# Kernel optimization log

Measured on AMD Instinct MI355X. Metric: run time of the kernel, lower is better.

Reference implementation:

```python
import jax, jax.numpy as jnp
import numpy as np

B, S, E, D, H = 32, 4096, 512, 512, 512


def setup_inputs() -> dict:
    key = jax.random.key(0)
    ks = jax.random.split(key, 7)
    scale = 1.0 / np.sqrt(H)
    return {
        "encoder_hiddens": jax.random.normal(ks[0], (B, S, E), dtype=jnp.float32),
        "decoder_hidden": jax.random.normal(ks[1], (B, D), dtype=jnp.float32),
        "W_enc": jax.random.uniform(ks[2], (H, E), jnp.float32, -scale, scale),
        "b_enc": jax.random.uniform(ks[3], (H,), jnp.float32, -scale, scale),
        "W_dec": jax.random.uniform(ks[4], (H, D), jnp.float32, -scale, scale),
        "b_dec": jax.random.uniform(ks[5], (H,), jnp.float32, -scale, scale),
        "v": jax.random.uniform(ks[6], (H,), jnp.float32, -scale, scale),
    }


def reference(encoder_hiddens, decoder_hidden, W_enc, b_enc, W_dec, b_dec, v):
    # Projections (the two small GEMMs of the original per-timestep loop, batched)
    enc_hs = jnp.einsum("bse,he->bsh", encoder_hiddens, W_enc) + b_enc  # [B,S,H]
    dec_h = decoder_hidden @ W_dec.T + b_dec                            # [B,H]

    # Ragged-length detection: the torch loop breaks at the first all-zero
    # projected encoder row; positions at/after that are excluded (cumulative AND).
    nonzero = jnp.any(enc_hs != 0, axis=-1)                             # [B,S]
    valid = jnp.cumprod(nonzero.astype(jnp.int32), axis=1).astype(bool)

    # Additive (Bahdanau) scores: v . tanh(enc_hs + dec_h)
    scores = jnp.einsum("h,bsh->bs", v, jnp.tanh(enc_hs + dec_h[:, None, :]))
    scores = jnp.where(valid, scores, -jnp.inf)
    attn = jax.nn.softmax(scores, axis=1)                               # [B,S]
    attn = jnp.where(valid, attn, 0.0)

    # Weighted sum of encoder states -> context vector [B,1,E]
    return jnp.sum(encoder_hiddens * attn[..., None], axis=1, keepdims=True)
```

## Files before the change

kernel.cpp:

```cpp
#include <hip/hip_runtime.h>
#include <hip/hip_bf16.h>

#define BATCH 32
#define SEQ   4096
#define EDIM  512
#define HDIM  512
#define NCHUNK 64
#define NBLK  (BATCH * NCHUNK)

typedef unsigned short u16;
typedef unsigned int   u32;

typedef __bf16 bf16x8 __attribute__((ext_vector_type(8)));
typedef float  f32x4  __attribute__((ext_vector_type(4)));

__device__ __forceinline__ u16 bf_rne(float x) {
    u32 u = __float_as_uint(x);
    u32 r = (u + 0x7fffu + ((u >> 16) & 1u)) >> 16;
    return (u16)r;
}
__device__ __forceinline__ u32 pack2(u16 lo, u16 hi) {
    return (u32)lo | ((u32)hi << 16);
}
__device__ __forceinline__ float tanh_fast(float x) {
    float e = __builtin_amdgcn_exp2f(x * 2.88539008177793f);
    return 1.0f - 2.0f * __builtin_amdgcn_rcpf(e + 1.0f);
}

__global__ void prep_kernel(const float* __restrict__ W_enc, uint4* __restrict__ wpack,
                            const float* __restrict__ dec, const float* __restrict__ Wd,
                            const float* __restrict__ b_enc, const float* __restrict__ b_dec,
                            float* __restrict__ dec_bias) {
    int bid = blockIdx.x;
    int t = threadIdx.x;
    if (bid < 4096) {
        int wave = t >> 6, lane = t & 63;
        int p = bid * 4 + wave;
        int b = p >> 9, h = p & 511;
        const float4* wr = reinterpret_cast<const float4*>(Wd)  + h * 128;
        const float4* dr = reinterpret_cast<const float4*>(dec) + b * 128;
        float4 w0 = wr[lane * 2], w1 = wr[lane * 2 + 1];
        float4 d0 = dr[lane * 2], d1 = dr[lane * 2 + 1];
        float s = w0.x * d0.x + w0.y * d0.y + w0.z * d0.z + w0.w * d0.w
                + w1.x * d1.x + w1.y * d1.y + w1.z * d1.z + w1.w * d1.w;
#pragma unroll
        for (int m = 1; m < 64; m <<= 1) s += __shfl_xor(s, m, 64);
        if (lane == 0) dec_bias[p] = s + b_dec[h] + b_enc[h];
    } else {
        int id   = (bid - 4096) * 256 + t;
        int nsub = id >> 10;
        int rem  = id & 1023;
        int kc   = rem >> 6;
        int lane = rem & 63;
        int row  = nsub * 16 + (lane & 15);
        int col  = kc * 32 + (lane >> 4) * 8;
        const float* src = W_enc + row * EDIM + col;
        uint4 o;
        o.x = pack2(bf_rne(src[0]), bf_rne(src[1]));
        o.y = pack2(bf_rne(src[2]), bf_rne(src[3]));
        o.z = pack2(bf_rne(src[4]), bf_rne(src[5]));
        o.w = pack2(bf_rne(src[6]), bf_rne(src[7]));
        wpack[id] = o;
    }
}

#define ASTRIDE 520

__global__ __launch_bounds__(256, 2) void fused_kernel(
    const float* __restrict__ X, const uint4* __restrict__ Wp,
    const float* __restrict__ bias, const float* __restrict__ v,
    float* __restrict__ cpart, float* __restrict__ mpart, float* __restrict__ lpart)
{
    __shared__ alignas(16) u16 Abuf[64 * ASTRIDE];
    __shared__ float sred[4][64];
    __shared__ float pbuf[64];

    const int tid  = threadIdx.x;
    const int wave = tid >> 6, lane = tid & 63;
    const int quad = lane >> 4, l15 = lane & 15;
    const int blk  = blockIdx.x;
    const int b    = blk >> 6;
    const long row0 = (long)blk * 64;
    const float4* X4 = reinterpret_cast<const float4*>(X + row0 * EDIM);

    const int r  = tid >> 2;
    const int c8 = tid & 3;

#pragma unroll
    for (int g = 0; g < 2; g++) {
        float4 st[16];
#pragma unroll
        for (int p = 0; p < 8; p++) {
            int piece = (g * 8 + p) * 4 + c8;
            st[2 * p]     = X4[r * 128 + piece * 2];
            st[2 * p + 1] = X4[r * 128 + piece * 2 + 1];
        }
#pragma unroll
        for (int p = 0; p < 8; p++) {
            int piece = (g * 8 + p) * 4 + c8;
            uint4 w;
            w.x = pack2(bf_rne(st[2 * p].x),     bf_rne(st[2 * p].y));
            w.y = pack2(bf_rne(st[2 * p].z),     bf_rne(st[2 * p].w));
            w.z = pack2(bf_rne(st[2 * p + 1].x), bf_rne(st[2 * p + 1].y));
            w.w = pack2(bf_rne(st[2 * p + 1].z), bf_rne(st[2 * p + 1].w));
            *reinterpret_cast<uint4*>(&Abuf[r * ASTRIDE + piece * 8]) = w;
        }
    }

    f32x4 acc[4][8] = {};
    __syncthreads();

    uint4 bcur[8], bnxt[8];
#pragma unroll
    for (int jj = 0; jj < 8; jj++)
        bcur[jj] = Wp[((wave * 8 + jj) * 16 + 0) * 64 + lane];

#pragma unroll
    for (int ks = 0; ks < 16; ks++) {
        if (ks < 15) {
#pragma unroll
            for (int jj = 0; jj < 8; jj++)
                bnxt[jj] = Wp[((wave * 8 + jj) * 16 + ks + 1) * 64 + lane];
        }
        bf16x8 af[4];
#pragma unroll
        for (int i = 0; i < 4; i++)
            af[i] = *reinterpret_cast<const bf16x8*>(
                &Abuf[(i * 16 + l15) * ASTRIDE + ks * 32 + quad * 8]);
#pragma unroll
        for (int jj = 0; jj < 8; jj++) {
            bf16x8 bfr = __builtin_bit_cast(bf16x8, bcur[jj]);
#pragma unroll
            for (int i = 0; i < 4; i++)
                acc[i][jj] = __builtin_amdgcn_mfma_f32_16x16x32_bf16(
                    af[i], bfr, acc[i][jj], 0, 0, 0);
        }
        if (ks < 15) {
#pragma unroll
            for (int jj = 0; jj < 8; jj++) bcur[jj] = bnxt[jj];
        }
    }

    float hb[8], hv[8];
#pragma unroll
    for (int jj = 0; jj < 8; jj++) {
        int h = wave * 128 + jj * 16 + l15;
        hb[jj] = bias[b * HDIM + h];
        hv[jj] = v[h];
    }
    float s_acc[16];
#pragma unroll
    for (int x = 0; x < 16; x++) s_acc[x] = 0.f;
#pragma unroll
    for (int i = 0; i < 4; i++)
#pragma unroll
        for (int jj = 0; jj < 8; jj++)
#pragma unroll
            for (int rr = 0; rr < 4; rr++)
                s_acc[i * 4 + rr] += hv[jj] * tanh_fast(acc[i][jj][rr] + hb[jj]);

#pragma unroll
    for (int m = 1; m < 16; m <<= 1)
#pragma unroll
        for (int x = 0; x < 16; x++)
            s_acc[x] += __shfl_xor(s_acc[x], m, 16);

    if (l15 == 0) {
#pragma unroll
        for (int x = 0; x < 16; x++) {
            int i = x >> 2, rr = x & 3;
            sred[wave][i * 16 + quad * 4 + rr] = s_acc[x];
        }
    }
    __syncthreads();

    if (tid < 64) {
        float sc = sred[0][tid] + sred[1][tid] + sred[2][tid] + sred[3][tid];
        float mx = sc;
#pragma unroll
        for (int m = 1; m < 64; m <<= 1) mx = fmaxf(mx, __shfl_xor(mx, m, 64));
        float p = __builtin_amdgcn_exp2f((sc - mx) * 1.44269504088896f);
        float l = p;
#pragma unroll
        for (int m = 1; m < 64; m <<= 1) l += __shfl_xor(l, m, 64);
        pbuf[tid] = p;
        if (tid == 0) { mpart[blk] = mx; lpart[blk] = l; }
    }
    __syncthreads();

    const float2* Xp = reinterpret_cast<const float2*>(X + row0 * EDIM) + tid;
    float ax0 = 0.f, ay0 = 0.f, ax1 = 0.f, ay1 = 0.f;
#pragma unroll 2
    for (int s = 0; s < 64; s += 8) {
        float2 x[8];
#pragma unroll
        for (int k = 0; k < 8; k++) x[k] = Xp[(s + k) * 256];
#pragma unroll
        for (int k = 0; k < 8; k += 2) {
            float w0 = pbuf[s + k], w1 = pbuf[s + k + 1];
            ax0 = fmaf(w0, x[k].x,     ax0);
            ay0 = fmaf(w0, x[k].y,     ay0);
            ax1 = fmaf(w1, x[k + 1].x, ax1);
            ay1 = fmaf(w1, x[k + 1].y, ay1);
        }
    }
    reinterpret_cast<float2*>(cpart)[blk * 256 + tid] =
        make_float2(ax0 + ax1, ay0 + ay1);
}

__global__ __launch_bounds__(256) void combine_k(const float* __restrict__ cpart,
                                                 const float* __restrict__ mpart,
                                                 const float* __restrict__ lpart,
                                                 float* __restrict__ out) {
    __shared__ float wbuf[64];
    __shared__ float linv_s;
    int b = blockIdx.x, t = threadIdx.x;
    if (t < 64) {
        float m = mpart[b * 64 + t];
        float M = m;
#pragma unroll
        for (int k = 1; k < 64; k <<= 1) M = fmaxf(M, __shfl_xor(M, k, 64));
        float w = __builtin_amdgcn_exp2f((m - M) * 1.44269504088896f);
        float lw = lpart[b * 64 + t] * w;
        float L = lw;
#pragma unroll
        for (int k = 1; k < 64; k <<= 1) L += __shfl_xor(L, k, 64);
        wbuf[t] = w;
        if (t == 0) linv_s = 1.0f / L;
    }
    __syncthreads();
    const float2* cp = reinterpret_cast<const float2*>(cpart) + (long)b * 64 * 256 + t;
    float ax = 0.f, ay = 0.f;
#pragma unroll 2
    for (int i = 0; i < 64; i += 8) {
        float2 x[8];
#pragma unroll
        for (int k = 0; k < 8; k++) x[k] = cp[(i + k) * 256];
#pragma unroll
        for (int k = 0; k < 8; k++) {
            float w = wbuf[i + k];
            ax = fmaf(w, x[k].x, ax);
            ay = fmaf(w, x[k].y, ay);
        }
    }
    float inv = linv_s;
    reinterpret_cast<float2*>(out)[b * 256 + t] = make_float2(ax * inv, ay * inv);
}

extern "C" void kernel_launch(void* const* d_in, const int* in_sizes, int n_in,
                              void* d_out, int out_size, void* d_ws, size_t ws_size,
                              hipStream_t stream) {
    const float* X      = (const float*)d_in[0];
    const float* dec    = (const float*)d_in[1];
    const float* W_enc  = (const float*)d_in[2];
    const float* b_enc  = (const float*)d_in[3];
    const float* W_dec  = (const float*)d_in[4];
    const float* b_dec  = (const float*)d_in[5];
    const float* v      = (const float*)d_in[6];
    float* out = (float*)d_out;

    char* ws = (char*)d_ws;
    uint4* wpack    = (uint4*)ws;
    float* dec_bias = (float*)(ws + (512 << 10));
    float* cpart    = (float*)(ws + (576 << 10));
    float* mpart    = (float*)(ws + (576 << 10) + (4096 << 10));
    float* lpart    = (float*)(ws + (576 << 10) + (4104 << 10));

    prep_kernel  <<<4224, 256, 0, stream>>>(W_enc, wpack, dec, W_dec, b_enc, b_dec,
                                            dec_bias);
    fused_kernel <<<NBLK, 256, 0, stream>>>(X, wpack, dec_bias, v, cpart, mpart, lpart);
    combine_k    <<<BATCH, 256, 0, stream>>>(cpart, mpart, lpart, out);
}
```

Baseline: 454.4 us.

## Use 512-thread blocks splitting H across eight waves to cut registers

The fused kernel now runs 512 threads per block (8 waves), and each wave computes 64 of the H columns instead of 128. That halves the accumulator and B-fragment registers, so launch bounds can ask for 4 blocks per SM. The double-buffered B prefetch is replaced by an in-loop reload after each MFMA group, and the context sum now uses one float per thread instead of float2. The aim is higher occupancy to hide memory latency, at the cost of less B prefetch depth and a larger cross-wave reduction.

```diff
diff --git a/kernel.cpp b/kernel.cpp
--- a/kernel.cpp
+++ b/kernel.cpp
@@ -66,13 +66,13 @@
 
 #define ASTRIDE 520
 
-__global__ __launch_bounds__(256, 2) void fused_kernel(
+__global__ __launch_bounds__(512, 4) void fused_kernel(
     const float* __restrict__ X, const uint4* __restrict__ Wp,
     const float* __restrict__ bias, const float* __restrict__ v,
     float* __restrict__ cpart, float* __restrict__ mpart, float* __restrict__ lpart)
 {
     __shared__ alignas(16) u16 Abuf[64 * ASTRIDE];
-    __shared__ float sred[4][64];
+    __shared__ float sred[8][64];
     __shared__ float pbuf[64];
 
     const int tid  = threadIdx.x;
@@ -83,68 +83,57 @@
     const long row0 = (long)blk * 64;
     const float4* X4 = reinterpret_cast<const float4*>(X + row0 * EDIM);
 
-    const int r  = tid >> 2;
-    const int c8 = tid & 3;
-
-#pragma unroll
-    for (int g = 0; g < 2; g++) {
-        float4 st[16];
-#pragma unroll
-        for (int p = 0; p < 8; p++) {
-            int piece = (g * 8 + p) * 4 + c8;
-            st[2 * p]     = X4[r * 128 + piece * 2];
-            st[2 * p + 1] = X4[r * 128 + piece * 2 + 1];
-        }
-#pragma unroll
-        for (int p = 0; p < 8; p++) {
-            int piece = (g * 8 + p) * 4 + c8;
-            uint4 w;
-            w.x = pack2(bf_rne(st[2 * p].x),     bf_rne(st[2 * p].y));
-            w.y = pack2(bf_rne(st[2 * p].z),     bf_rne(st[2 * p].w));
-            w.z = pack2(bf_rne(st[2 * p + 1].x), bf_rne(st[2 * p + 1].y));
-            w.w = pack2(bf_rne(st[2 * p + 1].z), bf_rne(st[2 * p + 1].w));
-            *reinterpret_cast<uint4*>(&Abuf[r * ASTRIDE + piece * 8]) = w;
-        }
-    }
-
-    f32x4 acc[4][8] = {};
-    __syncthreads();
-
-    uint4 bcur[8], bnxt[8];
-#pragma unroll
-    for (int jj = 0; jj < 8; jj++)
-        bcur[jj] = Wp[((wave * 8 + jj) * 16 + 0) * 64 + lane];
+    const int r  = tid >> 3;
+    const int c8 = tid & 7;
+
+    float4 st[16];
+#pragma unroll
+    for (int p = 0; p < 8; p++) {
+        int piece = p * 8 + c8;
+        st[2 * p]     = X4[r * 128 + piece * 2];
+        st[2 * p + 1] = X4[r * 128 + piece * 2 + 1];
+    }
+#pragma unroll
+    for (int p = 0; p < 8; p++) {
+        int piece = p * 8 + c8;
+        uint4 w;
+        w.x = pack2(bf_rne(st[2 * p].x),     bf_rne(st[2 * p].y));
+        w.y = pack2(bf_rne(st[2 * p].z),     bf_rne(st[2 * p].w));
+        w.z = pack2(bf_rne(st[2 * p + 1].x), bf_rne(st[2 * p + 1].y));
+        w.w = pack2(bf_rne(st[2 * p + 1].z), bf_rne(st[2 * p + 1].w));
+        *reinterpret_cast<uint4*>(&Abuf[r * ASTRIDE + piece * 8]) = w;
+    }
+
+    f32x4 acc[4][4] = {};
+    uint4 bcur[4];
+#pragma unroll
+    for (int jj = 0; jj < 4; jj++)
+        bcur[jj] = Wp[((wave * 4 + jj) * 16 + 0) * 64 + lane];
+    __syncthreads();
 
 #pragma unroll
     for (int ks = 0; ks < 16; ks++) {
-        if (ks < 15) {
-#pragma unroll
-            for (int jj = 0; jj < 8; jj++)
-                bnxt[jj] = Wp[((wave * 8 + jj) * 16 + ks + 1) * 64 + lane];
-        }
         bf16x8 af[4];
 #pragma unroll
         for (int i = 0; i < 4; i++)
             af[i] = *reinterpret_cast<const bf16x8*>(
                 &Abuf[(i * 16 + l15) * ASTRIDE + ks * 32 + quad * 8]);
 #pragma unroll
-        for (int jj = 0; jj < 8; jj++) {
+        for (int jj = 0; jj < 4; jj++) {
             bf16x8 bfr = __builtin_bit_cast(bf16x8, bcur[jj]);
 #pragma unroll
             for (int i = 0; i < 4; i++)
                 acc[i][jj] = __builtin_amdgcn_mfma_f32_16x16x32_bf16(
                     af[i], bfr, acc[i][jj], 0, 0, 0);
-        }
-        if (ks < 15) {
-#pragma unroll
-            for (int jj = 0; jj < 8; jj++) bcur[jj] = bnxt[jj];
-        }
-    }
-
-    float hb[8], hv[8];
-#pragma unroll
-    for (int jj = 0; jj < 8; jj++) {
-        int h = wave * 128 + jj * 16 + l15;
+            if (ks < 15)
+                bcur[jj] = Wp[((wave * 4 + jj) * 16 + ks + 1) * 64 + lane];
+        }
+    }
+
+    float hb[4], hv[4];
+#pragma unroll
+    for (int jj = 0; jj < 4; jj++) {
+        int h = wave * 64 + jj * 16 + l15;
         hb[jj] = bias[b * HDIM + h];
         hv[jj] = v[h];
     }
@@ -154,7 +143,7 @@
 #pragma unroll
     for (int i = 0; i < 4; i++)
 #pragma unroll
-        for (int jj = 0; jj < 8; jj++)
+        for (int jj = 0; jj < 4; jj++)
 #pragma unroll
             for (int rr = 0; rr < 4; rr++)
                 s_acc[i * 4 + rr] += hv[jj] * tanh_fast(acc[i][jj][rr] + hb[jj]);
@@ -175,7 +164,8 @@
     __syncthreads();
 
     if (tid < 64) {
-        float sc = sred[0][tid] + sred[1][tid] + sred[2][tid] + sred[3][tid];
+        float sc = sred[0][tid] + sred[1][tid] + sred[2][tid] + sred[3][tid]
+                 + sred[4][tid] + sred[5][tid] + sred[6][tid] + sred[7][tid];
         float mx = sc;
 #pragma unroll
         for (int m = 1; m < 64; m <<= 1) mx = fmaxf(mx, __shfl_xor(mx, m, 64));
@@ -188,24 +178,20 @@
     }
     __syncthreads();
 
-    const float2* Xp = reinterpret_cast<const float2*>(X + row0 * EDIM) + tid;
-    float ax0 = 0.f, ay0 = 0.f, ax1 = 0.f, ay1 = 0.f;
+    const float* Xc = X + row0 * EDIM + tid;
+    float a0 = 0.f, a1 = 0.f;
 #pragma unroll 2
     for (int s = 0; s < 64; s += 8) {
-        float2 x[8];
-#pragma unroll
-        for (int k = 0; k < 8; k++) x[k] = Xp[(s + k) * 256];
+        float x[8];
+#pragma unroll
+        for (int k = 0; k < 8; k++) x[k] = Xc[(s + k) * EDIM];
 #pragma unroll
         for (int k = 0; k < 8; k += 2) {
-            float w0 = pbuf[s + k], w1 = pbuf[s + k + 1];
-            ax0 = fmaf(w0, x[k].x,     ax0);
-            ay0 = fmaf(w0, x[k].y,     ay0);
-            ax1 = fmaf(w1, x[k + 1].x, ax1);
-            ay1 = fmaf(w1, x[k + 1].y, ay1);
-        }
-    }
-    reinterpret_cast<float2*>(cpart)[blk * 256 + tid] =
-        make_float2(ax0 + ax1, ay0 + ay1);
+            a0 = fmaf(pbuf[s + k],     x[k],     a0);
+            a1 = fmaf(pbuf[s + k + 1], x[k + 1], a1);
+        }
+    }
+    cpart[(long)blk * EDIM + tid] = a0 + a1;
 }
 
 __global__ __launch_bounds__(256) void combine_k(const float* __restrict__ cpart,
@@ -268,6 +254,6 @@
 
     prep_kernel  <<<4224, 256, 0, stream>>>(W_enc, wpack, dec, W_dec, b_enc, b_dec,
                                             dec_bias);
-    fused_kernel <<<NBLK, 256, 0, stream>>>(X, wpack, dec_bias, v, cpart, mpart, lpart);
+    fused_kernel <<<NBLK, 512, 0, stream>>>(X, wpack, dec_bias, v, cpart, mpart, lpart);
     combine_k    <<<BATCH, 256, 0, stream>>>(cpart, mpart, lpart, out);
 }
```

Result: no change. 462.4 us (+1.8%).
